# Kernel optimization log

Measured on AMD Instinct MI355X. Metric: run time of the kernel, lower is better.

## Reference

```python
import jax, jax.numpy as jnp
import numpy as np

N_ATOMS = 20000
N_EDGES = 200000
C = 64
N_BASIS = 8
R_CUT = 5.0
NORM_FACTOR = 10.0
EPS = 1e-6
# coupling paths (in_way, r_way, out_way) with out = in + r - 2k, all ways <= 2
# index: 0:(0,0,0) 1:(0,1,1) 2:(0,2,2) 3:(1,0,1) 4:(1,1,0) 5:(1,1,2) 6:(1,2,1) 7:(2,0,2) 8:(2,1,1) 9:(2,2,0) 10:(2,2,2)
N_COMBO = 11


def setup_inputs() -> dict:
    key = jax.random.key(0)
    ks = jax.random.split(key, 16)
    f32 = jnp.float32
    return {
        "node0": jax.random.normal(ks[0], (N_ATOMS, C), f32),
        "node1": jax.random.normal(ks[1], (N_ATOMS, C, 3), f32),
        "node2": jax.random.normal(ks[2], (N_ATOMS, C, 3, 3), f32),
        "edge0": jax.random.normal(ks[3], (N_EDGES, C), f32),
        "rij": jax.random.normal(ks[4], (N_EDGES, 3), f32),
        "idx_i": jax.random.randint(ks[5], (N_EDGES,), 0, N_ATOMS),
        "idx_j": jax.random.randint(ks[6], (N_EDGES,), 0, N_ATOMS),
        "rbf_w": jax.random.normal(ks[7], (N_COMBO, N_BASIS, C), f32) * 0.1,
        "si_w0": jax.random.normal(ks[8], (C, C), f32) / np.sqrt(C),
        "si_b0": jnp.zeros((C,), f32),
        "si_w1": jax.random.normal(ks[9], (C, C), f32) / np.sqrt(C),
        "si_w2": jax.random.normal(ks[10], (C, C), f32) / np.sqrt(C),
        "nl_w1": jax.random.normal(ks[11], (C,), f32) * 0.1,
        "nl_b1": jnp.zeros((C,), f32),
        "nl_w2": jax.random.normal(ks[12], (C,), f32) * 0.1,
        "nl_b2": jnp.zeros((C,), f32),
    }


def reference(node0, node1, node2, edge0, rij, rbf_w, si_w0, si_b0, si_w1, si_w2,
              nl_w1, nl_b1, nl_w2, nl_b2, idx_i, idx_j):
    # ---- radial filters: Gaussian RBF * cosine cutoff, mixed per coupling path ----
    d = jnp.linalg.norm(rij, axis=-1)                         # [E]
    rhat = rij / (d[:, None] + 1e-12)                          # [E,3]
    mu = jnp.linspace(0.0, R_CUT, N_BASIS)
    g = jnp.exp(-2.0 * (d[:, None] - mu) ** 2)                 # [E,B]
    fcut = 0.5 * (jnp.cos(jnp.pi * jnp.clip(d, 0.0, R_CUT) / R_CUT) + 1.0)
    rbf = g * fcut[:, None]                                    # [E,B]
    fc = jnp.einsum('eb,kbc->kec', rbf, rbf_w)                 # [K,E,C]
    # ---- filter tensors of r_way 1,2 (outer products of unit vector) ----
    T1 = rhat                                                  # [E,3]
    T2 = rhat[:, :, None] * rhat[:, None, :]                   # [E,3,3]
    # ---- GraphConvLayer (conv_mode='node_j'): gather neighbor features ----
    h0 = node0[idx_j]                                          # [E,C]
    h1 = node1[idx_j]                                          # [E,C,3]
    h2 = node2[idx_j]                                          # [E,C,3,3]
    m0 = (fc[0] * h0
          + fc[4] * jnp.einsum('ecx,ex->ec', h1, T1)
          + fc[9] * jnp.einsum('ecxy,exy->ec', h2, T2))
    m1 = (fc[1][:, :, None] * (h0[:, :, None] * T1[:, None, :])
          + fc[3][:, :, None] * h1
          + fc[6][:, :, None] * jnp.einsum('ecx,exy->ecy', h1, T2)
          + fc[8][:, :, None] * jnp.einsum('ecxy,ey->ecx', h2, T1))
    m2 = (fc[2][:, :, None, None] * (h0[:, :, None, None] * T2[:, None])
          + fc[5][:, :, None, None] * (h1[:, :, :, None] * T1[:, None, None, :])
          + fc[7][:, :, None, None] * h2
          + fc[10][:, :, None, None] * jnp.einsum('ecxy,eyz->ecxz', h2, T2))
    # ---- per-way scatter_add over idx_i, normalized ----
    n = node0.shape[0]
    a0 = jax.ops.segment_sum(m0, idx_i, num_segments=n) / NORM_FACTOR
    a1 = jax.ops.segment_sum(m1, idx_i, num_segments=n) / NORM_FACTOR
    a2 = jax.ops.segment_sum(m2, idx_i, num_segments=n) / NORM_FACTOR
    # ---- SelfInteractionLayer: per-way channel mixing (bias only for way 0) ----
    s0 = a0 @ si_w0 + si_b0
    s1 = jnp.einsum('ncx,cd->ndx', a1, si_w1)
    s2 = jnp.einsum('ncxy,cd->ndxy', a2, si_w2)
    # ---- NonLinearLayer: silu on scalars, norm-gated silu on higher ways ----
    r0 = jax.nn.silu(s0)
    nrm1 = jnp.sqrt(jnp.sum(s1 * s1, axis=-1) + EPS)
    r1 = s1 * jax.nn.silu(nrm1 * nl_w1 + nl_b1)[:, :, None]
    nrm2 = jnp.sqrt(jnp.sum(s2 * s2, axis=(-2, -1)) + EPS)
    r2 = s2 * jax.nn.silu(nrm2 * nl_w2 + nl_b2)[:, :, None, None]
    # ---- res_add with node_info; update_edge=False -> edge_info unchanged ----
    return (node0 + r0, node1 + r1, node2 + r2, edge0)
```

## Files before the change

kernel.cpp:

```cpp
#include <hip/hip_runtime.h>
#include <math.h>

#define N_ATOMS 20000
#define N_EDGES 200000
#define CH 64
#define NB 8
#define NK 11
#define ATOMS_PER_BLOCK 4
#define ATOM_BLOCKS (N_ATOMS / ATOMS_PER_BLOCK)
#define COPY_F4 (N_EDGES * CH / 4)
#define COPY_PER_BLOCK 1024
#define COPY_BLOCKS (COPY_F4 / COPY_PER_BLOCK)

#define WSTRIDE 44

typedef _Float16 h2 __attribute__((ext_vector_type(2)));
typedef __fp16  p2 __attribute__((ext_vector_type(2)));

union F2H { float f; h2 h; p2 p; unsigned int u; };

static __device__ __forceinline__ h2 pack_f16(float a, float b) {
    F2H u;
    u.p = __builtin_amdgcn_cvt_pkrtz(a, b);
    return u.h;
}

__global__ __launch_bounds__(256) void hist_kernel(
    const int* __restrict__ idx_i, int* __restrict__ counts)
{
    int e = blockIdx.x * blockDim.x + threadIdx.x;
    if (e >= N_EDGES) return;
    atomicAdd(&counts[idx_i[e]], 1);
}

__global__ __launch_bounds__(1024) void scan_kernel(
    const int* __restrict__ counts, int* __restrict__ offsets,
    int* __restrict__ cursor)
{
    __shared__ int part[1024];
    const int CHUNK = 20;
    int t = threadIdx.x;
    int beg = t * CHUNK;
    int s = 0;
    for (int k = 0; k < CHUNK; ++k) {
        int idx = beg + k;
        if (idx < N_ATOMS) s += counts[idx];
    }
    part[t] = s;
    __syncthreads();
    for (int off = 1; off < 1024; off <<= 1) {
        int v = (t >= off) ? part[t - off] : 0;
        __syncthreads();
        part[t] += v;
        __syncthreads();
    }
    int run = part[t] - s;
    for (int k = 0; k < CHUNK; ++k) {
        int idx = beg + k;
        if (idx < N_ATOMS) {
            offsets[idx] = run;
            cursor[idx] = run;
            run += counts[idx];
        }
    }
    if (t == 0) offsets[N_ATOMS] = N_EDGES;
}

__global__ __launch_bounds__(256) void scatter_geom_kernel(
    const float* __restrict__ rij, const int* __restrict__ idx_i,
    const int* __restrict__ idx_j, int* __restrict__ cursor,
    int* __restrict__ jlist, float4* __restrict__ ge4)
{
    int e = blockIdx.x * blockDim.x + threadIdx.x;
    if (e >= N_EDGES) return;

    float rx = rij[e * 3 + 0];
    float ry = rij[e * 3 + 1];
    float rz = rij[e * 3 + 2];
    float d = sqrtf(rx * rx + ry * ry + rz * rz);
    float inv = 1.0f / (d + 1e-12f);

    float dc = fminf(d, 5.0f);
    float fcut = 0.5f * (cosf(3.14159265358979323846f * dc * 0.2f) + 1.0f);

    float rbf[NB];
#pragma unroll
    for (int b = 0; b < NB; ++b) {
        float mu = (5.0f / 7.0f) * (float)b;
        float t = d - mu;
        rbf[b] = expf(-2.0f * t * t) * fcut;
    }

    int p = atomicAdd(&cursor[idx_i[e]], 1);
    jlist[p] = idx_j[e];
    ge4[p * 3 + 0] = make_float4(rx * inv, ry * inv, rz * inv, rbf[0]);
    ge4[p * 3 + 1] = make_float4(rbf[1], rbf[2], rbf[3], rbf[4]);
    ge4[p * 3 + 2] = make_float4(rbf[5], rbf[6], rbf[7], 0.f);
}

__global__ __launch_bounds__(256) void atom_fused_kernel(
    const float* __restrict__ node0, const float* __restrict__ node1,
    const float* __restrict__ node2,
    const int* __restrict__ jlist, const int* __restrict__ offsets,
    const float4* __restrict__ ge4, const float* __restrict__ rbf_w,
    const float* __restrict__ si_w0, const float* __restrict__ si_b0,
    const float* __restrict__ si_w1, const float* __restrict__ si_w2,
    const float* __restrict__ nl_w1, const float* __restrict__ nl_b1,
    const float* __restrict__ nl_w2, const float* __restrict__ nl_b2,
    float* __restrict__ out0, float* __restrict__ out1, float* __restrict__ out2,
    const float4* __restrict__ edge0_in, float4* __restrict__ edge0_out)
{
    int bid = blockIdx.x;

    if (bid >= ATOM_BLOCKS) {
        size_t base = (size_t)(bid - ATOM_BLOCKS) * COPY_PER_BLOCK;
#pragma unroll
        for (int k = 0; k < 4; ++k)
            edge0_out[base + k * 256 + threadIdx.x] =
                edge0_in[base + k * 256 + threadIdx.x];
        return;
    }

    __shared__ __align__(16) float wlds[CH * WSTRIDE];
    __shared__ float2 ab2[ATOMS_PER_BLOCK][CH][7];

    int wv = threadIdx.x >> 6;
    int c = threadIdx.x & 63;

    {
        for (int kd = wv; kd < WSTRIDE; kd += 4) {
            int k = kd >> 2, j = kd & 3;
            float w0 = rbf_w[(k * NB + 2 * j) * CH + c];
            float w1 = rbf_w[(k * NB + 2 * j + 1) * CH + c];
            F2H u;
            u.p = __builtin_amdgcn_cvt_pkrtz(w0, w1);
            wlds[c * WSTRIDE + kd] = u.f;
        }
    }
    __syncthreads();

    int n = bid * ATOMS_PER_BLOCK + wv;

    float a0 = 0.f;
    float a1[3] = {0.f, 0.f, 0.f};
    float a2[9] = {0.f, 0.f, 0.f, 0.f, 0.f, 0.f, 0.f, 0.f, 0.f};

    int beg = offsets[n];
    int end = offsets[n + 1];

    float4 g0, g1v, g2v;
    float h0 = 0.f, h1[3] = {0.f, 0.f, 0.f};
    float h2v[9] = {0.f, 0.f, 0.f, 0.f, 0.f, 0.f, 0.f, 0.f, 0.f};
    int jnx = 0;

    if (beg < end) {
        int j = jlist[beg];
        g0 = ge4[beg * 3 + 0];
        g1v = ge4[beg * 3 + 1];
        g2v = ge4[beg * 3 + 2];
        h0 = node0[(size_t)j * CH + c];
#pragma unroll
        for (int x = 0; x < 3; ++x) h1[x] = node1[((size_t)j * CH + c) * 3 + x];
#pragma unroll
        for (int q = 0; q < 9; ++q) h2v[q] = node2[((size_t)j * CH + c) * 9 + q];
        jnx = (beg + 1 < end) ? jlist[beg + 1] : 0;
    }

    for (int p = beg; p < end; ++p) {
        float rh[3] = {g0.x, g0.y, g0.z};
        float rbf[NB] = {g0.w, g1v.x, g1v.y, g1v.z, g1v.w, g2v.x, g2v.y, g2v.z};
        float ch0 = h0;
        float ch1[3] = {h1[0], h1[1], h1[2]};
        float ch2[9];
#pragma unroll
        for (int q = 0; q < 9; ++q) ch2[q] = h2v[q];

        if (p + 1 < end) {
            int j2 = jnx;
            g0 = ge4[(p + 1) * 3 + 0];
            g1v = ge4[(p + 1) * 3 + 1];
            g2v = ge4[(p + 1) * 3 + 2];
            h0 = node0[(size_t)j2 * CH + c];
#pragma unroll
            for (int x = 0; x < 3; ++x) h1[x] = node1[((size_t)j2 * CH + c) * 3 + x];
#pragma unroll
            for (int q = 0; q < 9; ++q) h2v[q] = node2[((size_t)j2 * CH + c) * 9 + q];
            jnx = (p + 2 < end) ? jlist[p + 2] : 0;
        }

        h2 rb[4];
        rb[0] = pack_f16(rbf[0], rbf[1]);
        rb[1] = pack_f16(rbf[2], rbf[3]);
        rb[2] = pack_f16(rbf[4], rbf[5]);
        rb[3] = pack_f16(rbf[6], rbf[7]);

        int cop = c;
        asm volatile("" : "+v"(cop));
        const float4* wp4 = reinterpret_cast<const float4*>(&wlds[cop * WSTRIDE]);

        float fc[NK];
#pragma unroll
        for (int k = 0; k < NK; ++k) {
            float4 w = wp4[k];
            F2H u0, u1_, u2, u3;
            u0.f = w.x; u1_.f = w.y; u2.f = w.z; u3.f = w.w;
            float s = __builtin_amdgcn_fdot2(rb[0], u0.h, 0.f, false);
            s = __builtin_amdgcn_fdot2(rb[1], u1_.h, s, false);
            s = __builtin_amdgcn_fdot2(rb[2], u2.h, s, false);
            fc[k] = __builtin_amdgcn_fdot2(rb[3], u3.h, s, false);
        }

        float u1 = ch1[0] * rh[0] + ch1[1] * rh[1] + ch1[2] * rh[2];
        float v2[3];
#pragma unroll
        for (int x = 0; x < 3; ++x)
            v2[x] = ch2[x * 3] * rh[0] + ch2[x * 3 + 1] * rh[1] + ch2[x * 3 + 2] * rh[2];
        float w2 = v2[0] * rh[0] + v2[1] * rh[1] + v2[2] * rh[2];

        a0 = fmaf(fc[0], ch0, a0);
        a0 = fmaf(fc[4], u1, a0);
        a0 = fmaf(fc[9], w2, a0);

        float c1 = fc[1] * ch0 + fc[6] * u1;
#pragma unroll
        for (int x = 0; x < 3; ++x)
            a1[x] += c1 * rh[x] + fc[3] * ch1[x] + fc[8] * v2[x];

#pragma unroll
        for (int x = 0; x < 3; ++x) {
            float cx = fc[2] * ch0 * rh[x] + fc[5] * ch1[x] + fc[10] * v2[x];
#pragma unroll
            for (int y = 0; y < 3; ++y)
                a2[x * 3 + y] += cx * rh[y] + fc[7] * ch2[x * 3 + y];
        }
    }

    const float SC = 0.1f;
    ab2[wv][c][0] = make_float2(a0 * SC, a1[0] * SC);
    ab2[wv][c][1] = make_float2(a1[1] * SC, a1[2] * SC);
    ab2[wv][c][2] = make_float2(a2[0] * SC, a2[1] * SC);
    ab2[wv][c][3] = make_float2(a2[2] * SC, a2[3] * SC);
    ab2[wv][c][4] = make_float2(a2[4] * SC, a2[5] * SC);
    ab2[wv][c][5] = make_float2(a2[6] * SC, a2[7] * SC);
    ab2[wv][c][6] = make_float2(a2[8] * SC, 0.f);

    __builtin_amdgcn_wave_barrier();

    float s0 = si_b0[c];
    float s1[3] = {0.f, 0.f, 0.f};
    float s2[9] = {0.f, 0.f, 0.f, 0.f, 0.f, 0.f, 0.f, 0.f, 0.f};

    for (int cc = 0; cc < CH; ++cc) {
        float2 q0 = ab2[wv][cc][0];
        float2 q1 = ab2[wv][cc][1];
        float2 q2 = ab2[wv][cc][2];
        float2 q3 = ab2[wv][cc][3];
        float2 q4 = ab2[wv][cc][4];
        float2 q5 = ab2[wv][cc][5];
        float2 q6 = ab2[wv][cc][6];
        float w0 = si_w0[cc * CH + c];
        float w1 = si_w1[cc * CH + c];
        float w2m = si_w2[cc * CH + c];
        s0 = fmaf(q0.x, w0, s0);
        s1[0] = fmaf(q0.y, w1, s1[0]);
        s1[1] = fmaf(q1.x, w1, s1[1]);
        s1[2] = fmaf(q1.y, w1, s1[2]);
        s2[0] = fmaf(q2.x, w2m, s2[0]);
        s2[1] = fmaf(q2.y, w2m, s2[1]);
        s2[2] = fmaf(q3.x, w2m, s2[2]);
        s2[3] = fmaf(q3.y, w2m, s2[3]);
        s2[4] = fmaf(q4.x, w2m, s2[4]);
        s2[5] = fmaf(q4.y, w2m, s2[5]);
        s2[6] = fmaf(q5.x, w2m, s2[6]);
        s2[7] = fmaf(q5.y, w2m, s2[7]);
        s2[8] = fmaf(q6.x, w2m, s2[8]);
    }

    float r0 = s0 / (1.0f + expf(-s0));

    float n1 = sqrtf(s1[0] * s1[0] + s1[1] * s1[1] + s1[2] * s1[2] + 1e-6f);
    float g1 = n1 * nl_w1[c] + nl_b1[c];
    float gate1 = g1 / (1.0f + expf(-g1));

    float n2sq = 1e-6f;
#pragma unroll
    for (int q = 0; q < 9; ++q) n2sq = fmaf(s2[q], s2[q], n2sq);
    float n2 = sqrtf(n2sq);
    float g2 = n2 * nl_w2[c] + nl_b2[c];
    float gate2 = g2 / (1.0f + expf(-g2));

    out0[(size_t)n * CH + c] = node0[(size_t)n * CH + c] + r0;
#pragma unroll
    for (int x = 0; x < 3; ++x)
        out1[((size_t)n * CH + c) * 3 + x] =
            node1[((size_t)n * CH + c) * 3 + x] + s1[x] * gate1;
#pragma unroll
    for (int q = 0; q < 9; ++q)
        out2[((size_t)n * CH + c) * 9 + q] =
            node2[((size_t)n * CH + c) * 9 + q] + s2[q] * gate2;
}

extern "C" void kernel_launch(void* const* d_in, const int* in_sizes, int n_in,
                              void* d_out, int out_size, void* d_ws, size_t ws_size,
                              hipStream_t stream) {
    const float* node0 = (const float*)d_in[0];
    const float* node1 = (const float*)d_in[1];
    const float* node2 = (const float*)d_in[2];
    const float* edge0 = (const float*)d_in[3];
    const float* rij   = (const float*)d_in[4];
    const int*   idx_i = (const int*)d_in[5];
    const int*   idx_j = (const int*)d_in[6];
    const float* rbf_w = (const float*)d_in[7];
    const float* si_w0 = (const float*)d_in[8];
    const float* si_b0 = (const float*)d_in[9];
    const float* si_w1 = (const float*)d_in[10];
    const float* si_w2 = (const float*)d_in[11];
    const float* nl_w1 = (const float*)d_in[12];
    const float* nl_b1 = (const float*)d_in[13];
    const float* nl_w2 = (const float*)d_in[14];
    const float* nl_b2 = (const float*)d_in[15];

    float* out = (float*)d_out;
    float* out0 = out;
    float* out1 = out + (size_t)N_ATOMS * CH;
    float* out2 = out1 + (size_t)N_ATOMS * CH * 3;
    float* oute = out2 + (size_t)N_ATOMS * CH * 9;

    char* ws = (char*)d_ws;
    int* counts  = (int*)ws;                              ws += N_ATOMS * sizeof(int);
    int* cursor  = (int*)ws;                              ws += N_ATOMS * sizeof(int);
    int* offsets = (int*)ws;                              ws += (N_ATOMS + 1) * sizeof(int);
    ws = (char*)(((size_t)ws + 15) & ~(size_t)15);
    int* jlist   = (int*)ws;                              ws += N_EDGES * sizeof(int);
    ws = (char*)(((size_t)ws + 15) & ~(size_t)15);
    float4* ge4  = (float4*)ws;

    hipMemsetAsync(counts, 0, N_ATOMS * sizeof(int), stream);

    hist_kernel<<<(N_EDGES + 255) / 256, 256, 0, stream>>>(idx_i, counts);

    scan_kernel<<<1, 1024, 0, stream>>>(counts, offsets, cursor);

    scatter_geom_kernel<<<(N_EDGES + 255) / 256, 256, 0, stream>>>(
        rij, idx_i, idx_j, cursor, jlist, ge4);

    atom_fused_kernel<<<ATOM_BLOCKS + COPY_BLOCKS, 256, 0, stream>>>(
        node0, node1, node2, jlist, offsets, ge4, rbf_w,
        si_w0, si_b0, si_w1, si_w2, nl_w1, nl_b1, nl_w2, nl_b2,
        out0, out1, out2,
        (const float4*)edge0, (float4*)oute);
}
```

Before: 212.4 us.

## Split self-interaction and nonlinearity epilogue into separate per-way kernels

The edge-accumulation kernel no longer does the per-atom channel mixing and gating. It writes the scaled aggregates into the output buffers in a channel-planar layout. Three new epilogue kernels, one per tensor way, then read the aggregates back and apply the 64x64 channel mix from weights held in registers. Each applies the silu or norm gate plus the residual in place, with each wave looping over many atoms. The aim is to cut register and LDS pressure and serial work in the main accumulation kernel, at the cost of an extra global round trip of all aggregates and three more launches.

```diff
diff --git a/kernel.cpp b/kernel.cpp
--- a/kernel.cpp
+++ b/kernel.cpp
@@ -14,16 +14,17 @@
 
 #define WSTRIDE 44
 
+#define E0_APW 64
+#define E0_BLOCKS 79
+#define E1_APW 16
+#define E1_BLOCKS 313
+#define E2_APW 8
+#define E2_BLOCKS 625
+
 typedef _Float16 h2 __attribute__((ext_vector_type(2)));
 typedef __fp16  p2 __attribute__((ext_vector_type(2)));
 
 union F2H { float f; h2 h; p2 p; unsigned int u; };
-
-static __device__ __forceinline__ h2 pack_f16(float a, float b) {
-    F2H u;
-    u.p = __builtin_amdgcn_cvt_pkrtz(a, b);
-    return u.h;
-}
 
 __global__ __launch_bounds__(256) void hist_kernel(
     const int* __restrict__ idx_i, int* __restrict__ counts)
@@ -98,15 +99,11 @@
     ge4[p * 3 + 2] = make_float4(rbf[5], rbf[6], rbf[7], 0.f);
 }
 
-__global__ __launch_bounds__(256) void atom_fused_kernel(
+__global__ __launch_bounds__(256) void edge_acc_kernel(
     const float* __restrict__ node0, const float* __restrict__ node1,
     const float* __restrict__ node2,
     const int* __restrict__ jlist, const int* __restrict__ offsets,
     const float4* __restrict__ ge4, const float* __restrict__ rbf_w,
-    const float* __restrict__ si_w0, const float* __restrict__ si_b0,
-    const float* __restrict__ si_w1, const float* __restrict__ si_w2,
-    const float* __restrict__ nl_w1, const float* __restrict__ nl_b1,
-    const float* __restrict__ nl_w2, const float* __restrict__ nl_b2,
     float* __restrict__ out0, float* __restrict__ out1, float* __restrict__ out2,
     const float4* __restrict__ edge0_in, float4* __restrict__ edge0_out)
 {
@@ -122,7 +119,6 @@
     }
 
     __shared__ __align__(16) float wlds[CH * WSTRIDE];
-    __shared__ float2 ab2[ATOMS_PER_BLOCK][CH][7];
 
     int wv = threadIdx.x >> 6;
     int c = threadIdx.x & 63;
@@ -189,10 +185,13 @@
         }
 
         h2 rb[4];
-        rb[0] = pack_f16(rbf[0], rbf[1]);
-        rb[1] = pack_f16(rbf[2], rbf[3]);
-        rb[2] = pack_f16(rbf[4], rbf[5]);
-        rb[3] = pack_f16(rbf[6], rbf[7]);
+        {
+            F2H u;
+            u.p = __builtin_amdgcn_cvt_pkrtz(rbf[0], rbf[1]); rb[0] = u.h;
+            u.p = __builtin_amdgcn_cvt_pkrtz(rbf[2], rbf[3]); rb[1] = u.h;
+            u.p = __builtin_amdgcn_cvt_pkrtz(rbf[4], rbf[5]); rb[2] = u.h;
+            u.p = __builtin_amdgcn_cvt_pkrtz(rbf[6], rbf[7]); rb[3] = u.h;
+        }
 
         int cop = c;
         asm volatile("" : "+v"(cop));
@@ -236,68 +235,118 @@
     }
 
     const float SC = 0.1f;
-    ab2[wv][c][0] = make_float2(a0 * SC, a1[0] * SC);
-    ab2[wv][c][1] = make_float2(a1[1] * SC, a1[2] * SC);
-    ab2[wv][c][2] = make_float2(a2[0] * SC, a2[1] * SC);
-    ab2[wv][c][3] = make_float2(a2[2] * SC, a2[3] * SC);
-    ab2[wv][c][4] = make_float2(a2[4] * SC, a2[5] * SC);
-    ab2[wv][c][5] = make_float2(a2[6] * SC, a2[7] * SC);
-    ab2[wv][c][6] = make_float2(a2[8] * SC, 0.f);
-
-    __builtin_amdgcn_wave_barrier();
-
-    float s0 = si_b0[c];
-    float s1[3] = {0.f, 0.f, 0.f};
-    float s2[9] = {0.f, 0.f, 0.f, 0.f, 0.f, 0.f, 0.f, 0.f, 0.f};
-
-    for (int cc = 0; cc < CH; ++cc) {
-        float2 q0 = ab2[wv][cc][0];
-        float2 q1 = ab2[wv][cc][1];
-        float2 q2 = ab2[wv][cc][2];
-        float2 q3 = ab2[wv][cc][3];
-        float2 q4 = ab2[wv][cc][4];
-        float2 q5 = ab2[wv][cc][5];
-        float2 q6 = ab2[wv][cc][6];
-        float w0 = si_w0[cc * CH + c];
-        float w1 = si_w1[cc * CH + c];
-        float w2m = si_w2[cc * CH + c];
-        s0 = fmaf(q0.x, w0, s0);
-        s1[0] = fmaf(q0.y, w1, s1[0]);
-        s1[1] = fmaf(q1.x, w1, s1[1]);
-        s1[2] = fmaf(q1.y, w1, s1[2]);
-        s2[0] = fmaf(q2.x, w2m, s2[0]);
-        s2[1] = fmaf(q2.y, w2m, s2[1]);
-        s2[2] = fmaf(q3.x, w2m, s2[2]);
-        s2[3] = fmaf(q3.y, w2m, s2[3]);
-        s2[4] = fmaf(q4.x, w2m, s2[4]);
-        s2[5] = fmaf(q4.y, w2m, s2[5]);
-        s2[6] = fmaf(q5.x, w2m, s2[6]);
-        s2[7] = fmaf(q5.y, w2m, s2[7]);
-        s2[8] = fmaf(q6.x, w2m, s2[8]);
-    }
-
-    float r0 = s0 / (1.0f + expf(-s0));
-
-    float n1 = sqrtf(s1[0] * s1[0] + s1[1] * s1[1] + s1[2] * s1[2] + 1e-6f);
-    float g1 = n1 * nl_w1[c] + nl_b1[c];
-    float gate1 = g1 / (1.0f + expf(-g1));
-
-    float n2sq = 1e-6f;
-#pragma unroll
-    for (int q = 0; q < 9; ++q) n2sq = fmaf(s2[q], s2[q], n2sq);
-    float n2 = sqrtf(n2sq);
-    float g2 = n2 * nl_w2[c] + nl_b2[c];
-    float gate2 = g2 / (1.0f + expf(-g2));
-
-    out0[(size_t)n * CH + c] = node0[(size_t)n * CH + c] + r0;
+    out0[(size_t)n * CH + c] = a0 * SC;
 #pragma unroll
     for (int x = 0; x < 3; ++x)
-        out1[((size_t)n * CH + c) * 3 + x] =
-            node1[((size_t)n * CH + c) * 3 + x] + s1[x] * gate1;
+        out1[(size_t)n * 192 + x * 64 + c] = a1[x] * SC;
 #pragma unroll
     for (int q = 0; q < 9; ++q)
-        out2[((size_t)n * CH + c) * 9 + q] =
-            node2[((size_t)n * CH + c) * 9 + q] + s2[q] * gate2;
+        out2[(size_t)n * 576 + q * 64 + c] = a2[q] * SC;
+}
+
+__global__ __launch_bounds__(256, 2) void epi0_kernel(
+    float* __restrict__ o0, const float* __restrict__ node0,
+    const float* __restrict__ si_w0, const float* __restrict__ si_b0)
+{
+    int wid = blockIdx.x * 4 + (threadIdx.x >> 6);
+    int c = threadIdx.x & 63;
+
+    float w0r[CH];
+#pragma unroll
+    for (int cc = 0; cc < CH; ++cc) w0r[cc] = si_w0[cc * CH + c];
+    float b0 = si_b0[c];
+
+    for (int t = 0; t < E0_APW; ++t) {
+        int n = wid * E0_APW + t;
+        if (n >= N_ATOMS) break;
+        const float* ap = o0 + (size_t)n * CH;
+
+        float p0 = 0.f, p1 = 0.f, p2s = 0.f, p3 = 0.f;
+#pragma unroll
+        for (int cc = 0; cc < CH; cc += 4) {
+            p0 = fmaf(ap[cc + 0], w0r[cc + 0], p0);
+            p1 = fmaf(ap[cc + 1], w0r[cc + 1], p1);
+            p2s = fmaf(ap[cc + 2], w0r[cc + 2], p2s);
+            p3 = fmaf(ap[cc + 3], w0r[cc + 3], p3);
+        }
+        float s0 = b0 + ((p0 + p1) + (p2s + p3));
+        float r0 = s0 / (1.0f + expf(-s0));
+        o0[(size_t)n * CH + c] = node0[(size_t)n * CH + c] + r0;
+    }
+}
+
+__global__ __launch_bounds__(256, 2) void epi1_kernel(
+    float* __restrict__ o1, const float* __restrict__ node1,
+    const float* __restrict__ si_w1,
+    const float* __restrict__ nl_w1, const float* __restrict__ nl_b1)
+{
+    int wid = blockIdx.x * 4 + (threadIdx.x >> 6);
+    int c = threadIdx.x & 63;
+
+    float w1r[CH];
+#pragma unroll
+    for (int cc = 0; cc < CH; ++cc) w1r[cc] = si_w1[cc * CH + c];
+    float nw = nl_w1[c], nb = nl_b1[c];
+
+    for (int t = 0; t < E1_APW; ++t) {
+        int n = wid * E1_APW + t;
+        if (n >= N_ATOMS) break;
+        const float* ap = o1 + (size_t)n * 192;
+
+        float s1[3] = {0.f, 0.f, 0.f};
+#pragma unroll
+        for (int x = 0; x < 3; ++x)
+#pragma unroll
+            for (int cc = 0; cc < CH; ++cc)
+                s1[x] = fmaf(ap[x * 64 + cc], w1r[cc], s1[x]);
+
+        float n1 = sqrtf(s1[0] * s1[0] + s1[1] * s1[1] + s1[2] * s1[2] + 1e-6f);
+        float g1 = n1 * nw + nb;
+        float gate1 = g1 / (1.0f + expf(-g1));
+#pragma unroll
+        for (int x = 0; x < 3; ++x)
+            o1[(size_t)n * 192 + c * 3 + x] =
+                node1[(size_t)n * 192 + c * 3 + x] + s1[x] * gate1;
+    }
+}
+
+__global__ __launch_bounds__(256, 2) void epi2_kernel(
+    float* __restrict__ o2, const float* __restrict__ node2,
+    const float* __restrict__ si_w2,
+    const float* __restrict__ nl_w2, const float* __restrict__ nl_b2)
+{
+    int wid = blockIdx.x * 4 + (threadIdx.x >> 6);
+    int c = threadIdx.x & 63;
+
+    float w2r[CH];
+#pragma unroll
+    for (int cc = 0; cc < CH; ++cc) w2r[cc] = si_w2[cc * CH + c];
+    float nw = nl_w2[c], nb = nl_b2[c];
+
+    for (int t = 0; t < E2_APW; ++t) {
+        int n = wid * E2_APW + t;
+        if (n >= N_ATOMS) break;
+        const float* ap = o2 + (size_t)n * 576;
+
+        float s2[9];
+#pragma unroll
+        for (int q = 0; q < 9; ++q) s2[q] = 0.f;
+#pragma unroll
+        for (int q = 0; q < 9; ++q)
+#pragma unroll
+            for (int cc = 0; cc < CH; ++cc)
+                s2[q] = fmaf(ap[q * 64 + cc], w2r[cc], s2[q]);
+
+        float n2sq = 1e-6f;
+#pragma unroll
+        for (int q = 0; q < 9; ++q) n2sq = fmaf(s2[q], s2[q], n2sq);
+        float g2 = sqrtf(n2sq) * nw + nb;
+        float gate2 = g2 / (1.0f + expf(-g2));
+#pragma unroll
+        for (int q = 0; q < 9; ++q)
+            o2[(size_t)n * 576 + c * 9 + q] =
+                node2[(size_t)n * 576 + c * 9 + q] + s2[q] * gate2;
+    }
 }
 
 extern "C" void kernel_launch(void* const* d_in, const int* in_sizes, int n_in,
@@ -344,9 +393,12 @@
     scatter_geom_kernel<<<(N_EDGES + 255) / 256, 256, 0, stream>>>(
         rij, idx_i, idx_j, cursor, jlist, ge4);
 
-    atom_fused_kernel<<<ATOM_BLOCKS + COPY_BLOCKS, 256, 0, stream>>>(
+    edge_acc_kernel<<<ATOM_BLOCKS + COPY_BLOCKS, 256, 0, stream>>>(
         node0, node1, node2, jlist, offsets, ge4, rbf_w,
-        si_w0, si_b0, si_w1, si_w2, nl_w1, nl_b1, nl_w2, nl_b2,
         out0, out1, out2,
         (const float4*)edge0, (float4*)oute);
-}
+
+    epi0_kernel<<<E0_BLOCKS, 256, 0, stream>>>(out0, node0, si_w0, si_b0);
+    epi1_kernel<<<E1_BLOCKS, 256, 0, stream>>>(out1, node1, si_w1, nl_w1, nl_b1);
+    epi2_kernel<<<E2_BLOCKS, 256, 0, stream>>>(out2, node2, si_w2, nl_w2, nl_b2);
+}
```

After: 401.0 us. 88.8% more time.
